# Kernel tuning notes

Measured on AMD Instinct MI355X. Metric: run time of the kernel, lower is better.

The kernel has to match this reference:

```python
import jax, jax.numpy as jnp
import numpy as np

NUM_EMB = 1024
EMB_DIM = 256
COMMIT = 0.25
EPS = 1e-12  # matches torch F.normalize eps


def _l2norm(x):
    return x / jnp.maximum(jnp.linalg.norm(x, axis=-1, keepdims=True), EPS)


def setup_inputs() -> dict:
    key = jax.random.key(0)
    k1, k2 = jax.random.split(key)
    inputs = jax.random.normal(k1, (64, 256, 32, 32), dtype=jnp.float32)
    weight = jax.random.uniform(k2, (NUM_EMB, EMB_DIM), dtype=jnp.float32,
                                minval=-1.0 / NUM_EMB, maxval=1.0 / NUM_EMB)
    return {"inputs": inputs, "weight": weight}


def reference(inputs, weight):
    B, D, H, W = inputs.shape
    x = jnp.transpose(inputs, (0, 2, 3, 1))           # [B,H,W,D]
    flat = x.reshape(-1, D)                           # [N,D]
    fn = _l2norm(flat)                                # normalized inputs
    wn = _l2norm(weight)                              # normalized codebook [K,D]
    # squared euclidean distances between unit vectors
    dist = (jnp.sum(fn * fn, axis=1, keepdims=True)
            + jnp.sum(wn * wn, axis=1)
            - 2.0 * fn @ wn.T)                        # [N,K]
    idx = jnp.argmin(dist, axis=1)                    # [N]
    quant = wn[idx].reshape(x.shape)                  # codebook gather == onehot @ wn
    inorm = fn.reshape(x.shape)
    e_loss = jnp.mean((jax.lax.stop_gradient(quant) - inorm) ** 2)
    q_loss = jnp.mean((quant - jax.lax.stop_gradient(inorm)) ** 2)
    loss = q_loss + COMMIT * e_loss
    quant_st = inorm + jax.lax.stop_gradient(quant - inorm)  # straight-through
    return loss, jnp.transpose(quant_st, (0, 3, 1, 2)), idx[:, None]
```

## Files before the change

kernel.cpp:

```cpp
#include <hip/hip_runtime.h>
#include <math.h>

#define NUM_EMB 1024
#define EMB_DIM 256
#define N_ROWS  65536
#define HW      1024
#define QUANT_OFF 1
#define IDX_OFF   (1 + 16777216)
#define LDA 272

typedef unsigned int uint;
typedef _Float16 f16x8 __attribute__((ext_vector_type(8)));
typedef float    f32x4 __attribute__((ext_vector_type(4)));

__device__ __forceinline__ uint umin2(uint a, uint b) { return a < b ? a : b; }
__device__ __forceinline__ uint umax2(uint a, uint b) { return a > b ? a : b; }

__device__ __forceinline__ void load_lds16(const _Float16* g, _Float16* l) {
  __builtin_amdgcn_global_load_lds(
      (const __attribute__((address_space(1))) unsigned int*)g,
      (__attribute__((address_space(3))) unsigned int*)l, 16, 0, 0);
}

__global__ __launch_bounds__(256)
void k_norm_w(const float* __restrict__ w, float* __restrict__ wn,
              _Float16* __restrict__ wh2, double* __restrict__ rinv) {
  const int k = blockIdx.x, t = threadIdx.x;
  const float v = w[(size_t)k * EMB_DIM + t];
  double s = (double)v * (double)v;
  for (int o = 32; o; o >>= 1) s += __shfl_down(s, o);
  __shared__ double ps[4];
  if ((t & 63) == 0) ps[t >> 6] = s;
  __syncthreads();
  const double tot = ps[0] + ps[1] + ps[2] + ps[3];
  const float nv = v / fmaxf((float)sqrt(tot), 1e-12f);
  wn[(size_t)k * EMB_DIM + t] = nv;
  const int chunk = k >> 8, cc = k & 255;
  const int ks = t >> 5, q = (t >> 3) & 3, e = t & 7;
  wh2[(size_t)chunk * 65536 + ks * 8192 + q * 2048 + cc * 8 + e] = (_Float16)nv;
  if (t == 0) rinv[k] = 1.0 / fmax(sqrt(tot), 1e-12);
}

__global__ __launch_bounds__(256)
void k_pass1(const float* __restrict__ x, const _Float16* __restrict__ wh2,
             uint* __restrict__ cand) {
  __shared__ __align__(16) _Float16 As[64 * LDA];
  __shared__ __align__(16) _Float16 Bs[8192];
  const int t = threadIdx.x;
  const int blk = blockIdx.x;
  const int b = blk >> 4;
  const int hw0 = (blk & 15) * 64;

  {
    const int lhw = t & 63;
    const int ph = t >> 6;
    const float* xb = x + (size_t)b * (EMB_DIM * HW) + hw0 + lhw;
#pragma unroll 8
    for (int j = 0; j < 64; ++j) {
      const int d = ph + j * 4;
      As[lhw * LDA + d] = (_Float16)xb[(size_t)d * HW];
    }
  }

  const int lane = t & 63;
  const int q = lane >> 4;
  const int l15 = lane & 15;
  const int w = t >> 6;

  uint t1[16], t2[16];
#pragma unroll
  for (int i = 0; i < 16; ++i) { t1[i] = 0u; t2[i] = 0u; }

  for (int c4 = 0; c4 < 4; ++c4) {
    f32x4 acc[4][4];
#pragma unroll
    for (int rt = 0; rt < 4; ++rt)
#pragma unroll
      for (int ct = 0; ct < 4; ++ct) acc[rt][ct] = (f32x4)0.f;

#pragma unroll 1
    for (int ks = 0; ks < 8; ++ks) {
      __syncthreads();
      {
        const _Float16* slab = wh2 + (size_t)c4 * 65536 + ks * 8192 + t * 8;
        _Float16* dst = &Bs[t * 8];
#pragma unroll
        for (int i = 0; i < 4; ++i)
          load_lds16(slab + i * 2048, dst + i * 2048);
      }
      __syncthreads();

      const f16x8 a0 = *(const f16x8*)&As[(0 * 16 + l15) * LDA + ks * 32 + q * 8];
      const f16x8 a1 = *(const f16x8*)&As[(1 * 16 + l15) * LDA + ks * 32 + q * 8];
      const f16x8 a2 = *(const f16x8*)&As[(2 * 16 + l15) * LDA + ks * 32 + q * 8];
      const f16x8 a3 = *(const f16x8*)&As[(3 * 16 + l15) * LDA + ks * 32 + q * 8];
      const f16x8 b0 = *(const f16x8*)&Bs[q * 2048 + (w * 64 +  0 + l15) * 8];
      const f16x8 b1 = *(const f16x8*)&Bs[q * 2048 + (w * 64 + 16 + l15) * 8];
      const f16x8 b2 = *(const f16x8*)&Bs[q * 2048 + (w * 64 + 32 + l15) * 8];
      const f16x8 b3 = *(const f16x8*)&Bs[q * 2048 + (w * 64 + 48 + l15) * 8];
      acc[0][0] = __builtin_amdgcn_mfma_f32_16x16x32_f16(a0, b0, acc[0][0], 0, 0, 0);
      acc[1][0] = __builtin_amdgcn_mfma_f32_16x16x32_f16(a1, b0, acc[1][0], 0, 0, 0);
      acc[2][0] = __builtin_amdgcn_mfma_f32_16x16x32_f16(a2, b0, acc[2][0], 0, 0, 0);
      acc[3][0] = __builtin_amdgcn_mfma_f32_16x16x32_f16(a3, b0, acc[3][0], 0, 0, 0);
      acc[0][1] = __builtin_amdgcn_mfma_f32_16x16x32_f16(a0, b1, acc[0][1], 0, 0, 0);
      acc[1][1] = __builtin_amdgcn_mfma_f32_16x16x32_f16(a1, b1, acc[1][1], 0, 0, 0);
      acc[2][1] = __builtin_amdgcn_mfma_f32_16x16x32_f16(a2, b1, acc[2][1], 0, 0, 0);
      acc[3][1] = __builtin_amdgcn_mfma_f32_16x16x32_f16(a3, b1, acc[3][1], 0, 0, 0);
      acc[0][2] = __builtin_amdgcn_mfma_f32_16x16x32_f16(a0, b2, acc[0][2], 0, 0, 0);
      acc[1][2] = __builtin_amdgcn_mfma_f32_16x16x32_f16(a1, b2, acc[1][2], 0, 0, 0);
      acc[2][2] = __builtin_amdgcn_mfma_f32_16x16x32_f16(a2, b2, acc[2][2], 0, 0, 0);
      acc[3][2] = __builtin_amdgcn_mfma_f32_16x16x32_f16(a3, b2, acc[3][2], 0, 0, 0);
      acc[0][3] = __builtin_amdgcn_mfma_f32_16x16x32_f16(a0, b3, acc[0][3], 0, 0, 0);
      acc[1][3] = __builtin_amdgcn_mfma_f32_16x16x32_f16(a1, b3, acc[1][3], 0, 0, 0);
      acc[2][3] = __builtin_amdgcn_mfma_f32_16x16x32_f16(a2, b3, acc[2][3], 0, 0, 0);
      acc[3][3] = __builtin_amdgcn_mfma_f32_16x16x32_f16(a3, b3, acc[3][3], 0, 0, 0);
    }

#pragma unroll
    for (int ct = 0; ct < 4; ++ct) {
      const uint idxv = (uint)(c4 * 256 + w * 64 + ct * 16 + l15);
#pragma unroll
      for (int rt = 0; rt < 4; ++rt)
#pragma unroll
        for (int r = 0; r < 4; ++r) {
          const float v = fmaxf(acc[rt][ct][r], 0.0f);
          const uint key = (__float_as_uint(v) & 0xFFFFFC00u) | idxv;
          const int slot = rt * 4 + r;
          const uint lo = umin2(key, t1[slot]);
          t1[slot] = umax2(key, t1[slot]);
          t2[slot] = umax2(t2[slot], lo);
        }
    }
  }

  __syncthreads();
  uint* keys = (uint*)As;
#pragma unroll
  for (int slot = 0; slot < 16; ++slot) {
    const int rt = slot >> 2, r = slot & 3;
    const int row = rt * 16 + q * 4 + r;
    const int col = w * 32 + l15 * 2;
    keys[row * 128 + col] = t1[slot];
    keys[row * 128 + col + 1] = t2[slot];
  }
  __syncthreads();
  {
    const int row = t >> 2, seg = t & 3;
    uint s1 = 0, s2 = 0;
#pragma unroll
    for (int i = 0; i < 8; ++i) {
      const int ii = (i + t) & 7;
      const uint4 k4 = *(const uint4*)&keys[row * 128 + seg * 32 + ii * 4];
      const uint kk[4] = {k4.x, k4.y, k4.z, k4.w};
#pragma unroll
      for (int e = 0; e < 4; ++e) {
        const uint lo = umin2(kk[e], s1);
        s1 = umax2(kk[e], s1);
        s2 = umax2(s2, lo);
      }
    }
    __syncthreads();
    keys[t * 2] = s1;
    keys[t * 2 + 1] = s2;
  }
  __syncthreads();
  if (t < 64) {
    uint c0 = 0, c1 = 0, c2 = 0, c3 = 0;
#pragma unroll
    for (int i = 0; i < 8; ++i) {
      const uint k = keys[t * 8 + i];
      const uint n0 = umin2(c0, k); c0 = umax2(c0, k);
      const uint n1 = umin2(c1, n0); c1 = umax2(c1, n0);
      const uint n2 = umin2(c2, n1); c2 = umax2(c2, n1);
      c3 = umax2(c3, n2);
    }
    uint4 o; o.x = c0; o.y = c1; o.z = c2; o.w = c3;
    *(uint4*)&cand[(size_t)(blk * 64 + t) * 4] = o;
  }
}

#define XSTR 257
__global__ __launch_bounds__(256)
void k_finish(const float* __restrict__ x, const float* __restrict__ w,
              const float* __restrict__ wn, const double* __restrict__ rinv,
              const uint* __restrict__ cand, float* __restrict__ out) {
  __shared__ float smem[256 * 33];
  __shared__ double lsum[4];
  const int t = threadIdx.x;
  const int blk = blockIdx.x;
  const int b = blk >> 5;
  const int hw0 = (blk & 31) * 32;

  {
    const int r = t & 31, dp = t >> 5;
    const float* xb = x + (size_t)b * (EMB_DIM * HW) + hw0 + r;
#pragma unroll
    for (int j = 0; j < 32; ++j) {
      const int d = dp * 32 + j;
      smem[r * XSTR + d] = xb[(size_t)d * HW];
    }
  }
  __syncthreads();

  const int row = t >> 3;
  const int li = t & 7;
  const int n0 = blk * 32 + row;
  const uint4 ck = *(const uint4*)&cand[(size_t)n0 * 4];
  const uint cv[4] = {ck.x, ck.y, ck.z, ck.w};

  float xf[32];
#pragma unroll
  for (int k = 0; k < 8; ++k)
#pragma unroll
    for (int e = 0; e < 4; ++e)
      xf[k * 4 + e] = smem[row * XSTR + k * 32 + li * 4 + e];
  __syncthreads();

  double sxx = 0.0;
#pragma unroll
  for (int i = 0; i < 32; ++i) sxx = fma((double)xf[i], (double)xf[i], sxx);

  double sj[4];
#pragma unroll
  for (int j = 0; j < 4; ++j) {
    const int c = (int)(cv[j] & 1023u);
    const float* wr = w + (size_t)c * EMB_DIM;
    double s = 0.0;
#pragma unroll
    for (int k = 0; k < 8; ++k) {
      const float4 w4 = *(const float4*)&wr[k * 32 + li * 4];
      const float wv[4] = {w4.x, w4.y, w4.z, w4.w};
#pragma unroll
      for (int e = 0; e < 4; ++e)
        s = fma((double)xf[k * 4 + e], (double)wv[e], s);
    }
    sj[j] = s;
  }

#pragma unroll
  for (int o = 4; o; o >>= 1) {
    sxx += __shfl_down(sxx, o);
#pragma unroll
    for (int j = 0; j < 4; ++j) sj[j] += __shfl_down(sj[j], o);
  }

  double dmin = 0.0;
  int cw = 0;
  if (li == 0) {
    double qbest = -1e300; cw = 1 << 30;
#pragma unroll
    for (int j = 0; j < 4; ++j) {
      const int c = (int)(cv[j] & 1023u);
      const double qj = sj[j] * rinv[c];
      if (qj > qbest || (qj == qbest && c < cw)) { qbest = qj; cw = c; }
    }
    dmin = 2.0 - 2.0 * qbest / fmax(sqrt(sxx), 1e-12);
    out[IDX_OFF + n0] = (float)cw;
  }
  cw = __shfl(cw, (t & 63) & ~7);

  double v = dmin;
  v += __shfl_down(v, 32);
  v += __shfl_down(v, 16);
  v += __shfl_down(v, 8);
  if ((t & 63) == 0) lsum[t >> 6] = v;
  __syncthreads();
  if (t == 0)
    atomicAdd(out, (float)(1.25 * (lsum[0] + lsum[1] + lsum[2] + lsum[3]) / 16777216.0));

  {
    const float* wr = wn + (size_t)cw * EMB_DIM;
#pragma unroll
    for (int k = 0; k < 8; ++k) {
      const int d0 = k * 32 + li * 4;
      const float4 w4 = *(const float4*)&wr[d0];
      smem[(d0 + 0) * 33 + row] = w4.x;
      smem[(d0 + 1) * 33 + row] = w4.y;
      smem[(d0 + 2) * 33 + row] = w4.z;
      smem[(d0 + 3) * 33 + row] = w4.w;
    }
  }
  __syncthreads();
  {
    const int hw4 = (t & 7) * 4, dbase = t >> 3;
    float* qout = out + QUANT_OFF + (size_t)b * (EMB_DIM * HW) + hw0;
#pragma unroll
    for (int jj = 0; jj < 8; ++jj) {
      const int d = jj * 32 + dbase;
      float4 v4;
      v4.x = smem[d * 33 + hw4 + 0];
      v4.y = smem[d * 33 + hw4 + 1];
      v4.z = smem[d * 33 + hw4 + 2];
      v4.w = smem[d * 33 + hw4 + 3];
      *(float4*)&qout[(size_t)d * HW + hw4] = v4;
    }
  }
}

extern "C" void kernel_launch(void* const* d_in, const int* in_sizes, int n_in,
                              void* d_out, int out_size, void* d_ws, size_t ws_size,
                              hipStream_t stream) {
  const float* x = (const float*)d_in[0];
  const float* w = (const float*)d_in[1];
  float* out = (float*)d_out;

  char* ws = (char*)d_ws;
  float*     wn   = (float*)ws;
  _Float16*  wh2  = (_Float16*)(ws + 1048576);
  double*    rinv = (double*)(ws + 1048576 + 524288);
  uint*      cand = (uint*)(ws + 1048576 + 524288 + 8192);

  hipMemsetAsync(d_out, 0, sizeof(float), stream);
  hipLaunchKernelGGL(k_norm_w, dim3(NUM_EMB), dim3(256), 0, stream, w, wn, wh2, rinv);
  hipLaunchKernelGGL(k_pass1, dim3(N_ROWS / 64), dim3(256), 0, stream, x, wh2, cand);
  hipLaunchKernelGGL(k_finish, dim3(N_ROWS / 32), dim3(256), 0, stream, x, w, wn, rinv, cand, out);
}
```

Before: 213.8 us.

## Double-buffer codebook slabs in LDS and vectorize the input tile fill

The codebook slab staging in k_pass1 now uses two LDS buffers. The next slab's global-to-LDS load is issued before the current slab's MFMAs, and the loop needs only one barrier per step instead of two. The input tile is now converted and written to LDS as 8-wide f16 vectors, with the row pitch cut from 272 to 264 halves. The running top-2 update uses a single v_med3_u32 in place of the min/max pair. These changes aim to hide codebook load latency and cut barrier and LDS store overhead, at the cost of more LDS and reliance on the barrier to wait for the async loads.

New measurement: 203.8 us. -4.7%, faster.

```diff
diff --git a/kernel.cpp b/kernel.cpp
--- a/kernel.cpp
+++ b/kernel.cpp
@@ -7,7 +7,7 @@
 #define HW      1024
 #define QUANT_OFF 1
 #define IDX_OFF   (1 + 16777216)
-#define LDA 272
+#define LDA 264
 
 typedef unsigned int uint;
 typedef _Float16 f16x8 __attribute__((ext_vector_type(8)));
@@ -15,6 +15,12 @@
 
 __device__ __forceinline__ uint umin2(uint a, uint b) { return a < b ? a : b; }
 __device__ __forceinline__ uint umax2(uint a, uint b) { return a > b ? a : b; }
+
+__device__ __forceinline__ uint umed3(uint a, uint b, uint c) {
+  uint d;
+  asm("v_med3_u32 %0, %1, %2, %3" : "=v"(d) : "v"(a), "v"(b), "v"(c));
+  return d;
+}
 
 __device__ __forceinline__ void load_lds16(const _Float16* g, _Float16* l) {
   __builtin_amdgcn_global_load_lds(
@@ -45,20 +51,32 @@
 void k_pass1(const float* __restrict__ x, const _Float16* __restrict__ wh2,
              uint* __restrict__ cand) {
   __shared__ __align__(16) _Float16 As[64 * LDA];
-  __shared__ __align__(16) _Float16 Bs[8192];
+  __shared__ __align__(16) _Float16 Bs[2][8192];
   const int t = threadIdx.x;
   const int blk = blockIdx.x;
   const int b = blk >> 4;
   const int hw0 = (blk & 15) * 64;
 
   {
+    const _Float16* slab = wh2 + (size_t)t * 8;
+    _Float16* dst = &Bs[0][t * 8];
+#pragma unroll
+    for (int i = 0; i < 4; ++i)
+      load_lds16(slab + i * 2048, dst + i * 2048);
+  }
+
+  {
     const int lhw = t & 63;
     const int ph = t >> 6;
     const float* xb = x + (size_t)b * (EMB_DIM * HW) + hw0 + lhw;
-#pragma unroll 8
-    for (int j = 0; j < 64; ++j) {
-      const int d = ph + j * 4;
-      As[lhw * LDA + d] = (_Float16)xb[(size_t)d * HW];
+#pragma unroll
+    for (int jp = 0; jp < 8; ++jp) {
+      const int d0 = ph * 64 + jp * 8;
+      f16x8 v;
+#pragma unroll
+      for (int e = 0; e < 8; ++e)
+        v[e] = (_Float16)xb[(size_t)(d0 + e) * HW];
+      *(f16x8*)&As[lhw * LDA + d0] = v;
     }
   }
 
@@ -71,6 +89,9 @@
 #pragma unroll
   for (int i = 0; i < 16; ++i) { t1[i] = 0u; t2[i] = 0u; }
 
+  __syncthreads();
+
+  int cur = 0;
   for (int c4 = 0; c4 < 4; ++c4) {
     f32x4 acc[4][4];
 #pragma unroll
@@ -80,24 +101,24 @@
 
 #pragma unroll 1
     for (int ks = 0; ks < 8; ++ks) {
-      __syncthreads();
-      {
-        const _Float16* slab = wh2 + (size_t)c4 * 65536 + ks * 8192 + t * 8;
-        _Float16* dst = &Bs[t * 8];
+      const int s = c4 * 8 + ks;
+      if (s < 31) {
+        const int sn = s + 1;
+        const _Float16* slab = wh2 + (size_t)(sn >> 3) * 65536 + (sn & 7) * 8192 + t * 8;
+        _Float16* dst = &Bs[cur ^ 1][t * 8];
 #pragma unroll
         for (int i = 0; i < 4; ++i)
           load_lds16(slab + i * 2048, dst + i * 2048);
       }
-      __syncthreads();
 
       const f16x8 a0 = *(const f16x8*)&As[(0 * 16 + l15) * LDA + ks * 32 + q * 8];
       const f16x8 a1 = *(const f16x8*)&As[(1 * 16 + l15) * LDA + ks * 32 + q * 8];
       const f16x8 a2 = *(const f16x8*)&As[(2 * 16 + l15) * LDA + ks * 32 + q * 8];
       const f16x8 a3 = *(const f16x8*)&As[(3 * 16 + l15) * LDA + ks * 32 + q * 8];
-      const f16x8 b0 = *(const f16x8*)&Bs[q * 2048 + (w * 64 +  0 + l15) * 8];
-      const f16x8 b1 = *(const f16x8*)&Bs[q * 2048 + (w * 64 + 16 + l15) * 8];
-      const f16x8 b2 = *(const f16x8*)&Bs[q * 2048 + (w * 64 + 32 + l15) * 8];
-      const f16x8 b3 = *(const f16x8*)&Bs[q * 2048 + (w * 64 + 48 + l15) * 8];
+      const f16x8 b0 = *(const f16x8*)&Bs[cur][q * 2048 + (w * 64 +  0 + l15) * 8];
+      const f16x8 b1 = *(const f16x8*)&Bs[cur][q * 2048 + (w * 64 + 16 + l15) * 8];
+      const f16x8 b2 = *(const f16x8*)&Bs[cur][q * 2048 + (w * 64 + 32 + l15) * 8];
+      const f16x8 b3 = *(const f16x8*)&Bs[cur][q * 2048 + (w * 64 + 48 + l15) * 8];
       acc[0][0] = __builtin_amdgcn_mfma_f32_16x16x32_f16(a0, b0, acc[0][0], 0, 0, 0);
       acc[1][0] = __builtin_amdgcn_mfma_f32_16x16x32_f16(a1, b0, acc[1][0], 0, 0, 0);
       acc[2][0] = __builtin_amdgcn_mfma_f32_16x16x32_f16(a2, b0, acc[2][0], 0, 0, 0);
@@ -114,6 +135,9 @@
       acc[1][3] = __builtin_amdgcn_mfma_f32_16x16x32_f16(a1, b3, acc[1][3], 0, 0, 0);
       acc[2][3] = __builtin_amdgcn_mfma_f32_16x16x32_f16(a2, b3, acc[2][3], 0, 0, 0);
       acc[3][3] = __builtin_amdgcn_mfma_f32_16x16x32_f16(a3, b3, acc[3][3], 0, 0, 0);
+
+      __syncthreads();
+      cur ^= 1;
     }
 
 #pragma unroll
@@ -126,9 +150,8 @@
           const float v = fmaxf(acc[rt][ct][r], 0.0f);
           const uint key = (__float_as_uint(v) & 0xFFFFFC00u) | idxv;
           const int slot = rt * 4 + r;
-          const uint lo = umin2(key, t1[slot]);
+          t2[slot] = umed3(key, t1[slot], t2[slot]);
           t1[slot] = umax2(key, t1[slot]);
-          t2[slot] = umax2(t2[slot], lo);
         }
     }
   }
@@ -154,9 +177,8 @@
       const uint kk[4] = {k4.x, k4.y, k4.z, k4.w};
 #pragma unroll
       for (int e = 0; e < 4; ++e) {
-        const uint lo = umin2(kk[e], s1);
+        s2 = umed3(kk[e], s1, s2);
         s1 = umax2(kk[e], s1);
-        s2 = umax2(s2, lo);
       }
     }
     __syncthreads();
```
